# Kernel tuning notes

Measured on AMD Instinct MI355X. Metric: run time of the kernel, lower is better.

## Reference

```python
import jax, jax.numpy as jnp
import numpy as np

N = 100000      # num nodes
E = 1600000     # num edges (avg degree 16)
F_IN = 256      # num_node_features
HID = 128       # hid_dim
C = 16          # num_classes


def gcn_conv(x, W, b, src, dst, num_nodes):
    # Linear transform first (PyG GCNConv transforms then aggregates)
    h = x @ W  # [N, out]
    # Symmetric normalization with self-loops already included in src/dst
    ones = jnp.ones_like(dst, dtype=h.dtype)
    deg = jax.ops.segment_sum(ones, dst, num_segments=num_nodes)  # in-degree incl. self-loop
    dinv = jnp.where(deg > 0, jax.lax.rsqrt(deg), 0.0)
    norm = dinv[src] * dinv[dst]                 # [E+N]
    msg = h[src] * norm[:, None]                 # gather + scale
    out = jax.ops.segment_sum(msg, dst, num_segments=num_nodes)  # scatter-add
    return out + b


def setup_inputs() -> dict:
    key = jax.random.key(0)
    k = jax.random.split(key, 4)
    x = jax.random.normal(k[0], (N, F_IN), dtype=jnp.float32)
    edge_index = jax.random.randint(k[1], (2, E), 0, N, dtype=jnp.int32)
    W1 = jax.random.normal(k[2], (F_IN, HID), dtype=jnp.float32) * (1.0 / np.sqrt(F_IN))
    b1 = jnp.zeros((HID,), dtype=jnp.float32)
    W2 = jax.random.normal(k[3], (HID, C), dtype=jnp.float32) * (1.0 / np.sqrt(HID))
    b2 = jnp.zeros((C,), dtype=jnp.float32)
    return {"x": x, "edge_index": edge_index, "W1": W1, "b1": b1, "W2": W2, "b2": b2}


def reference(x, edge_index, W1, b1, W2, b2):
    num_nodes = x.shape[0]
    loop = jnp.arange(num_nodes, dtype=edge_index.dtype)
    src = jnp.concatenate([edge_index[0], loop])  # add self-loops
    dst = jnp.concatenate([edge_index[1], loop])
    h = gcn_conv(x, W1, b1, src, dst, num_nodes)
    h = jax.nn.relu(h)
    # F.dropout(training=self.training): identity in eval mode
    out = gcn_conv(h, W2, b2, src, dst, num_nodes)
    return out
```

## Files before the change

### kernel.cpp

```cpp
#include <hip/hip_runtime.h>
#include <cstddef>

#define CAP 48
#define NBUILD 4096

typedef short short8 __attribute__((ext_vector_type(8)));
typedef float floatx4 __attribute__((ext_vector_type(4)));

__device__ inline float b2f_lo(unsigned int u) {
  union { unsigned int i; float f; } c;
  c.i = u << 16;
  return c.f;
}
__device__ inline float b2f_hi(unsigned int u) {
  union { unsigned int i; float f; } c;
  c.i = u & 0xFFFF0000u;
  return c.f;
}
__device__ inline unsigned short f2b(float f) {
  union { float f; unsigned int i; } c;
  c.f = f;
  unsigned int u = c.i;
  unsigned int r = (u + 0x7FFFu + ((u >> 16) & 1u)) >> 16;
  return (unsigned short)r;
}
__device__ inline float dinv_of(int c) { return rsqrtf((float)(c + 1)); }

__global__ void k_prep(int* __restrict__ cnt, int N,
                       const float* __restrict__ W1, unsigned short* __restrict__ W1T) {
  int i = blockIdx.x * 256 + threadIdx.x;
  if (i < N) cnt[i] = 0;
  if (i < 256 * 128) {
    int k = i >> 7, n = i & 127;
    W1T[n * 256 + k] = f2b(W1[i]);
  }
}

__global__ __launch_bounds__(256) void k_build_gemm1(
    const int* __restrict__ src, const int* __restrict__ dst, int E, int N,
    int* __restrict__ cnt, int* __restrict__ bucket,
    const float* __restrict__ X, const unsigned short* __restrict__ W1T,
    unsigned short* __restrict__ H1, int M, int gblocks, int total) {
  __shared__ unsigned short As[64 * 40];
  __shared__ unsigned short Bs[128 * 40];

  const unsigned int idx = blockIdx.x;
  const unsigned int gBefore = (idx * (unsigned int)gblocks) / (unsigned int)total;
  const unsigned int gAfter = ((idx + 1) * (unsigned int)gblocks) / (unsigned int)total;
  const bool isGemm = (gAfter > gBefore);

  if (!isGemm) {
    const int bi = (int)(idx - gBefore);
    const int g = bi & 7;
    const int S = (N + 7) >> 3;
    const int lo = g * S;
    const int hi = min(N, lo + S);
    const int tb = (bi >> 3) * 256 + (int)threadIdx.x;
    const int T = (NBUILD >> 3) * 256;
    const int E4 = E & ~3;

    for (int i0 = tb * 4; i0 < E4; i0 += T * 4) {
      int4 d4 = *(const int4*)(dst + i0);
      int4 s4 = *(const int4*)(src + i0);
      int p0 = CAP, p1 = CAP, p2 = CAP, p3 = CAP;
      if (d4.x >= lo && d4.x < hi) p0 = atomicAdd(&cnt[d4.x], 1);
      if (d4.y >= lo && d4.y < hi) p1 = atomicAdd(&cnt[d4.y], 1);
      if (d4.z >= lo && d4.z < hi) p2 = atomicAdd(&cnt[d4.z], 1);
      if (d4.w >= lo && d4.w < hi) p3 = atomicAdd(&cnt[d4.w], 1);
      if (p0 < CAP) bucket[(size_t)d4.x * CAP + p0] = s4.x;
      if (p1 < CAP) bucket[(size_t)d4.y * CAP + p1] = s4.y;
      if (p2 < CAP) bucket[(size_t)d4.z * CAP + p2] = s4.z;
      if (p3 < CAP) bucket[(size_t)d4.w * CAP + p3] = s4.w;
    }
    if (tb < E - E4) {
      int i = E4 + tb;
      int d = dst[i], s = src[i];
      if (d >= lo && d < hi) {
        int pos = atomicAdd(&cnt[d], 1);
        if (pos < CAP) bucket[(size_t)d * CAP + pos] = s;
      }
    }
    return;
  }

  const int bid = (int)gBefore;
  const int tid = threadIdx.x;
  const int wave = tid >> 6;
  const int lane = tid & 63;
  const int quad = lane >> 4;
  const int l16 = lane & 15;
  const int row0 = bid * 64;
  const int n0 = wave * 32;

  floatx4 acc[4][2];
#pragma unroll
  for (int r = 0; r < 4; r++)
#pragma unroll
    for (int c = 0; c < 2; c++) acc[r][c] = (floatx4){0.f, 0.f, 0.f, 0.f};

  for (int k0 = 0; k0 < 256; k0 += 32) {
    {
      int r = tid >> 2;
      int q = tid & 3;
      int gr = row0 + r;
      float4 v0 = make_float4(0.f, 0.f, 0.f, 0.f), v1 = v0;
      if (gr < M) {
        const float4* xp = (const float4*)(X + (size_t)gr * 256 + k0 + q * 8);
        v0 = xp[0];
        v1 = xp[1];
      }
      unsigned short tmp[8];
      tmp[0] = f2b(v0.x); tmp[1] = f2b(v0.y); tmp[2] = f2b(v0.z); tmp[3] = f2b(v0.w);
      tmp[4] = f2b(v1.x); tmp[5] = f2b(v1.y); tmp[6] = f2b(v1.z); tmp[7] = f2b(v1.w);
      *(uint4*)(As + r * 40 + q * 8) = *(const uint4*)(tmp);
    }
    {
      int n = tid >> 1;
      int half = (tid & 1) * 16;
      const uint4* wp = (const uint4*)(W1T + (size_t)n * 256 + k0 + half);
      uint4 w0 = wp[0];
      uint4 w1 = wp[1];
      unsigned short* p = Bs + n * 40 + half;
      *(uint4*)(p) = w0;
      *(uint4*)(p + 8) = w1;
    }
    __syncthreads();

    short8 afr[4], bfr[2];
#pragma unroll
    for (int r = 0; r < 4; r++)
      afr[r] = *(const short8*)(As + (r * 16 + l16) * 40 + quad * 8);
#pragma unroll
    for (int c = 0; c < 2; c++)
      bfr[c] = *(const short8*)(Bs + (n0 + c * 16 + l16) * 40 + quad * 8);
#pragma unroll
    for (int r = 0; r < 4; r++)
#pragma unroll
      for (int c = 0; c < 2; c++)
        acc[r][c] = __builtin_amdgcn_mfma_f32_16x16x32_bf16(afr[r], bfr[c], acc[r][c], 0, 0, 0);
    __syncthreads();
  }

#pragma unroll
  for (int r = 0; r < 4; r++) {
#pragma unroll
    for (int c = 0; c < 2; c++) {
      int col = n0 + c * 16 + l16;
#pragma unroll
      for (int i = 0; i < 4; i++) {
        int gr = row0 + r * 16 + quad * 4 + i;
        if (gr < M) H1[(size_t)gr * 128 + col] = f2b(acc[r][c][i]);
      }
    }
  }
}

__global__ __launch_bounds__(256) void k_agg1g2(const unsigned short* __restrict__ H1,
                                                const int* __restrict__ cnt,
                                                const int* __restrict__ bucket,
                                                const float* __restrict__ b1,
                                                const float* __restrict__ W2,
                                                unsigned short* __restrict__ H2, int N) {
  __shared__ float Ws[16 * 130];
  {
    int t = threadIdx.x;
    if (t < 128) {
      const float4* s4 = (const float4*)(W2 + t * 16);
      float4 w0 = s4[0], w1 = s4[1], w2v = s4[2], w3 = s4[3];
      float* d = Ws + (t >> 3) * 130 + (t & 7) * 16;
      d[0] = w0.x;  d[1] = w0.y;  d[2] = w0.z;  d[3] = w0.w;
      d[4] = w1.x;  d[5] = w1.y;  d[6] = w1.z;  d[7] = w1.w;
      d[8] = w2v.x; d[9] = w2v.y; d[10] = w2v.z; d[11] = w2v.w;
      d[12] = w3.x; d[13] = w3.y; d[14] = w3.z; d[15] = w3.w;
    }
  }
  __syncthreads();

  const int lane = threadIdx.x & 15;
  const int node = blockIdx.x * 16 + (threadIdx.x >> 4);
  if (node >= N) return;
  const int cn = cnt[node];
  const float di = dinv_of(cn);
  const float wself = di * di;
  const int deg = min(cn, CAP);
  const int* bk = bucket + (size_t)node * CAP;

  int idx0 = (lane < deg) ? bk[lane] : 0;
  int idx1 = (lane + 16 < deg) ? bk[lane + 16] : 0;
  int idx2 = (lane + 32 < deg) ? bk[lane + 32] : 0;
  float dv0 = (lane < deg) ? dinv_of(cnt[idx0]) : 0.f;
  float dv1 = (lane + 16 < deg) ? dinv_of(cnt[idx1]) : 0.f;
  float dv2 = (lane + 32 < deg) ? dinv_of(cnt[idx2]) : 0.f;

  uint4 hs = ((const uint4*)(H1 + (size_t)node * 128))[lane];
  float a0 = b2f_lo(hs.x) * wself, a1 = b2f_hi(hs.x) * wself;
  float a2 = b2f_lo(hs.y) * wself, a3 = b2f_hi(hs.y) * wself;
  float a4 = b2f_lo(hs.z) * wself, a5 = b2f_hi(hs.z) * wself;
  float a6 = b2f_lo(hs.w) * wself, a7 = b2f_hi(hs.w) * wself;
  float c0 = 0.f, c1 = 0.f, c2 = 0.f, c3 = 0.f, c4 = 0.f, c5 = 0.f, c6 = 0.f, c7 = 0.f;

  for (int j = 0; j < deg; j += 4) {
    int b = j >> 4;
    int idxB = (b == 0) ? idx0 : ((b == 1) ? idx1 : idx2);
    float dvB = (b == 0) ? dv0 : ((b == 1) ? dv1 : dv2);
    int base = j & 15;
    int s0 = __shfl(idxB, base + 0, 16);
    int s1 = __shfl(idxB, base + 1, 16);
    int s2 = __shfl(idxB, base + 2, 16);
    int s3 = __shfl(idxB, base + 3, 16);
    float w0 = __shfl(dvB, base + 0, 16) * di;
    float w1 = __shfl(dvB, base + 1, 16) * di;
    float w2 = __shfl(dvB, base + 2, 16) * di;
    float w3 = __shfl(dvB, base + 3, 16) * di;
    uint4 v0 = ((const uint4*)(H1 + (size_t)s0 * 128))[lane];
    uint4 v1 = ((const uint4*)(H1 + (size_t)s1 * 128))[lane];
    uint4 v2 = ((const uint4*)(H1 + (size_t)s2 * 128))[lane];
    uint4 v3 = ((const uint4*)(H1 + (size_t)s3 * 128))[lane];
    a0 += b2f_lo(v0.x) * w0; a1 += b2f_hi(v0.x) * w0;
    a2 += b2f_lo(v0.y) * w0; a3 += b2f_hi(v0.y) * w0;
    a4 += b2f_lo(v0.z) * w0; a5 += b2f_hi(v0.z) * w0;
    a6 += b2f_lo(v0.w) * w0; a7 += b2f_hi(v0.w) * w0;
    c0 += b2f_lo(v1.x) * w1; c1 += b2f_hi(v1.x) * w1;
    c2 += b2f_lo(v1.y) * w1; c3 += b2f_hi(v1.y) * w1;
    c4 += b2f_lo(v1.z) * w1; c5 += b2f_hi(v1.z) * w1;
    c6 += b2f_lo(v1.w) * w1; c7 += b2f_hi(v1.w) * w1;
    a0 += b2f_lo(v2.x) * w2; a1 += b2f_hi(v2.x) * w2;
    a2 += b2f_lo(v2.y) * w2; a3 += b2f_hi(v2.y) * w2;
    a4 += b2f_lo(v2.z) * w2; a5 += b2f_hi(v2.z) * w2;
    a6 += b2f_lo(v2.w) * w2; a7 += b2f_hi(v2.w) * w2;
    a0 += b2f_lo(v3.x) * w3; a1 += b2f_hi(v3.x) * w3;
    a2 += b2f_lo(v3.y) * w3; a3 += b2f_hi(v3.y) * w3;
    a4 += b2f_lo(v3.z) * w3; a5 += b2f_hi(v3.z) * w3;
    a6 += b2f_lo(v3.w) * w3; a7 += b2f_hi(v3.w) * w3;
  }
  a0 += c0; a1 += c1; a2 += c2; a3 += c3;
  a4 += c4; a5 += c5; a6 += c6; a7 += c7;

  float4 bb0 = ((const float4*)b1)[lane * 2];
  float4 bb1 = ((const float4*)b1)[lane * 2 + 1];
  float av[8];
  av[0] = fmaxf(a0 + bb0.x, 0.f); av[1] = fmaxf(a1 + bb0.y, 0.f);
  av[2] = fmaxf(a2 + bb0.z, 0.f); av[3] = fmaxf(a3 + bb0.w, 0.f);
  av[4] = fmaxf(a4 + bb1.x, 0.f); av[5] = fmaxf(a5 + bb1.y, 0.f);
  av[6] = fmaxf(a6 + bb1.z, 0.f); av[7] = fmaxf(a7 + bb1.w, 0.f);

  float2 p2[8];
#pragma unroll
  for (int c = 0; c < 8; c++) p2[c] = make_float2(0.f, 0.f);
  const float* wl = Ws + lane * 130;
#pragma unroll
  for (int i = 0; i < 8; i++) {
    const float a = av[i];
    const float2* wr = (const float2*)(wl + i * 16);
#pragma unroll
    for (int c = 0; c < 8; c++) {
      float2 wv = wr[c];
      p2[c].x += a * wv.x;
      p2[c].y += a * wv.y;
    }
  }
  float p[16];
#pragma unroll
  for (int c = 0; c < 8; c++) { p[2 * c] = p2[c].x; p[2 * c + 1] = p2[c].y; }

  float k8[8];
  {
    const bool hi = (lane & 8) != 0;
#pragma unroll
    for (int i = 0; i < 8; i++) {
      float keep = hi ? p[8 + i] : p[i];
      float send = hi ? p[i] : p[8 + i];
      k8[i] = keep + __shfl_xor(send, 8, 16);
    }
  }
  float k4[4];
  {
    const bool hi = (lane & 4) != 0;
#pragma unroll
    for (int i = 0; i < 4; i++) {
      float keep = hi ? k8[4 + i] : k8[i];
      float send = hi ? k8[i] : k8[4 + i];
      k4[i] = keep + __shfl_xor(send, 4, 16);
    }
  }
  float k2[2];
  {
    const bool hi = (lane & 2) != 0;
#pragma unroll
    for (int i = 0; i < 2; i++) {
      float keep = hi ? k4[2 + i] : k4[i];
      float send = hi ? k4[i] : k4[2 + i];
      k2[i] = keep + __shfl_xor(send, 2, 16);
    }
  }
  float v;
  {
    const bool hi = (lane & 1) != 0;
    float keep = hi ? k2[1] : k2[0];
    float send = hi ? k2[0] : k2[1];
    v = keep + __shfl_xor(send, 1, 16);
  }
  H2[(size_t)node * 16 + lane] = f2b(v);
}

__global__ __launch_bounds__(256) void k_agg2(const unsigned short* __restrict__ H2,
                                              const int* __restrict__ cnt,
                                              const int* __restrict__ bucket,
                                              const float* __restrict__ b2,
                                              float* __restrict__ out, int N) {
  const int half = threadIdx.x & 1;
  const int node = blockIdx.x * 128 + (threadIdx.x >> 1);
  if (node >= N) return;
  const int cn = cnt[node];
  const float di = dinv_of(cn);
  const float wself = di * di;
  const int deg = min(cn, CAP);
  const int* bk = bucket + (size_t)node * CAP;

  uint4 h = ((const uint4*)(H2 + (size_t)node * 16))[half];
  float a0 = b2f_lo(h.x) * wself, a1 = b2f_hi(h.x) * wself;
  float a2 = b2f_lo(h.y) * wself, a3 = b2f_hi(h.y) * wself;
  float a4 = b2f_lo(h.z) * wself, a5 = b2f_hi(h.z) * wself;
  float a6 = b2f_lo(h.w) * wself, a7 = b2f_hi(h.w) * wself;

  for (int j = 0; j < deg; j += 4) {
    int4 s4 = *(const int4*)(bk + j);
    int s0 = s4.x;
    int s1 = (j + 1 < deg) ? s4.y : 0;
    int s2 = (j + 2 < deg) ? s4.z : 0;
    int s3 = (j + 3 < deg) ? s4.w : 0;
    float w0 = dinv_of(cnt[s0]) * di;
    float w1 = (j + 1 < deg) ? dinv_of(cnt[s1]) * di : 0.f;
    float w2 = (j + 2 < deg) ? dinv_of(cnt[s2]) * di : 0.f;
    float w3 = (j + 3 < deg) ? dinv_of(cnt[s3]) * di : 0.f;
    uint4 v0 = ((const uint4*)(H2 + (size_t)s0 * 16))[half];
    uint4 v1 = ((const uint4*)(H2 + (size_t)s1 * 16))[half];
    uint4 v2 = ((const uint4*)(H2 + (size_t)s2 * 16))[half];
    uint4 v3 = ((const uint4*)(H2 + (size_t)s3 * 16))[half];
    a0 += b2f_lo(v0.x) * w0 + b2f_lo(v1.x) * w1 + b2f_lo(v2.x) * w2 + b2f_lo(v3.x) * w3;
    a1 += b2f_hi(v0.x) * w0 + b2f_hi(v1.x) * w1 + b2f_hi(v2.x) * w2 + b2f_hi(v3.x) * w3;
    a2 += b2f_lo(v0.y) * w0 + b2f_lo(v1.y) * w1 + b2f_lo(v2.y) * w2 + b2f_lo(v3.y) * w3;
    a3 += b2f_hi(v0.y) * w0 + b2f_hi(v1.y) * w1 + b2f_hi(v2.y) * w2 + b2f_hi(v3.y) * w3;
    a4 += b2f_lo(v0.z) * w0 + b2f_lo(v1.z) * w1 + b2f_lo(v2.z) * w2 + b2f_lo(v3.z) * w3;
    a5 += b2f_hi(v0.z) * w0 + b2f_hi(v1.z) * w1 + b2f_hi(v2.z) * w2 + b2f_hi(v3.z) * w3;
    a6 += b2f_lo(v0.w) * w0 + b2f_lo(v1.w) * w1 + b2f_lo(v2.w) * w2 + b2f_lo(v3.w) * w3;
    a7 += b2f_hi(v0.w) * w0 + b2f_hi(v1.w) * w1 + b2f_hi(v2.w) * w2 + b2f_hi(v3.w) * w3;
  }

  float4 bb0 = ((const float4*)b2)[half * 2];
  float4 bb1 = ((const float4*)b2)[half * 2 + 1];
  float4 o0 = make_float4(a0 + bb0.x, a1 + bb0.y, a2 + bb0.z, a3 + bb0.w);
  float4 o1 = make_float4(a4 + bb1.x, a5 + bb1.y, a6 + bb1.z, a7 + bb1.w);
  ((float4*)(out + (size_t)node * 16))[half * 2] = o0;
  ((float4*)(out + (size_t)node * 16))[half * 2 + 1] = o1;
}


extern "C" void kernel_launch(void* const* d_in, const int* in_sizes, int n_in,
                              void* d_out, int out_size, void* d_ws, size_t ws_size,
                              hipStream_t stream) {
  const float* x  = (const float*)d_in[0];
  const int* eidx = (const int*)d_in[1];
  const float* W1 = (const float*)d_in[2];
  const float* b1 = (const float*)d_in[3];
  const float* W2 = (const float*)d_in[4];
  const float* b2 = (const float*)d_in[5];
  float* out = (float*)d_out;

  const int HID = in_sizes[3];
  const int F   = in_sizes[2] / HID;
  const int N   = in_sizes[0] / F;
  const int E   = in_sizes[1] / 2;
  (void)n_in; (void)out_size; (void)ws_size;

  const int* src = eidx;
  const int* dst = eidx + E;

  char* base = (char*)d_ws;
  size_t off = 0;
  auto alloc = [&](size_t bytes) -> char* {
    char* p = base + off;
    off = (off + bytes + 255) & ~(size_t)255;
    return p;
  };
  int*            cnt    = (int*)alloc((size_t)N * 4);
  int*            bucket = (int*)alloc((size_t)N * CAP * 4);
  unsigned short* w1t    = (unsigned short*)alloc((size_t)256 * 128 * 2);
  unsigned short* h1     = (unsigned short*)alloc((size_t)N * 128 * 2);
  unsigned short* h2     = (unsigned short*)alloc((size_t)N * 16 * 2);

  const int nbN = (N + 255) / 256;
  const int gblocks = (N + 63) / 64;
  const int total = NBUILD + gblocks;

  hipLaunchKernelGGL(k_prep, dim3(nbN), dim3(256), 0, stream, cnt, N, W1, w1t);
  hipLaunchKernelGGL(k_build_gemm1, dim3(total), dim3(256), 0, stream,
                     src, dst, E, N, cnt, bucket, x, w1t, h1, N, gblocks, total);
  hipLaunchKernelGGL(k_agg1g2, dim3((N + 15) / 16), dim3(256), 0, stream, h1, cnt, bucket,
                     b1, W2, h2, N);
  hipLaunchKernelGGL(k_agg2, dim3((N + 127) / 128), dim3(256), 0, stream, h2, cnt, bucket,
                     b2, out, N);
}
```

Baseline: 329.7 us.

## Drop range-partitioned bucket build; split layer-2 neighbor loop across lane pairs

The edge-bucketing part of the fused build/GEMM kernel no longer runs 8 passes over all edges with each pass filtering a destination range. Each thread now handles one group of four edges and issues atomics for all of them, which cuts redundant edge reads but gives up the locality of atomics and bucket writes within a range. The layer-2 aggregation now uses four threads per node instead of two: two parities split the neighbor list and their sums are combined with a shuffle. This doubles the grid and adds memory parallelism per node.

```diff
diff --git a/kernel.cpp b/kernel.cpp
--- a/kernel.cpp
+++ b/kernel.cpp
@@ -2,7 +2,6 @@
 #include <cstddef>
 
 #define CAP 48
-#define NBUILD 4096
 
 typedef short short8 __attribute__((ext_vector_type(8)));
 typedef float floatx4 __attribute__((ext_vector_type(4)));
@@ -51,31 +50,23 @@
 
   if (!isGemm) {
     const int bi = (int)(idx - gBefore);
-    const int g = bi & 7;
-    const int S = (N + 7) >> 3;
-    const int lo = g * S;
-    const int hi = min(N, lo + S);
-    const int tb = (bi >> 3) * 256 + (int)threadIdx.x;
-    const int T = (NBUILD >> 3) * 256;
-    const int E4 = E & ~3;
-
-    for (int i0 = tb * 4; i0 < E4; i0 += T * 4) {
+    const int tb = bi * 256 + (int)threadIdx.x;
+    const int i0 = tb * 4;
+    if (i0 >= E) return;
+    if (i0 + 3 < E) {
       int4 d4 = *(const int4*)(dst + i0);
       int4 s4 = *(const int4*)(src + i0);
-      int p0 = CAP, p1 = CAP, p2 = CAP, p3 = CAP;
-      if (d4.x >= lo && d4.x < hi) p0 = atomicAdd(&cnt[d4.x], 1);
-      if (d4.y >= lo && d4.y < hi) p1 = atomicAdd(&cnt[d4.y], 1);
-      if (d4.z >= lo && d4.z < hi) p2 = atomicAdd(&cnt[d4.z], 1);
-      if (d4.w >= lo && d4.w < hi) p3 = atomicAdd(&cnt[d4.w], 1);
+      int p0 = atomicAdd(&cnt[d4.x], 1);
+      int p1 = atomicAdd(&cnt[d4.y], 1);
+      int p2 = atomicAdd(&cnt[d4.z], 1);
+      int p3 = atomicAdd(&cnt[d4.w], 1);
       if (p0 < CAP) bucket[(size_t)d4.x * CAP + p0] = s4.x;
       if (p1 < CAP) bucket[(size_t)d4.y * CAP + p1] = s4.y;
       if (p2 < CAP) bucket[(size_t)d4.z * CAP + p2] = s4.z;
       if (p3 < CAP) bucket[(size_t)d4.w * CAP + p3] = s4.w;
-    }
-    if (tb < E - E4) {
-      int i = E4 + tb;
-      int d = dst[i], s = src[i];
-      if (d >= lo && d < hi) {
+    } else {
+      for (int i = i0; i < E; ++i) {
+        int d = dst[i], s = src[i];
         int pos = atomicAdd(&cnt[d], 1);
         if (pos < CAP) bucket[(size_t)d * CAP + pos] = s;
       }
@@ -308,8 +299,10 @@
                                               const int* __restrict__ bucket,
                                               const float* __restrict__ b2,
                                               float* __restrict__ out, int N) {
-  const int half = threadIdx.x & 1;
-  const int node = blockIdx.x * 128 + (threadIdx.x >> 1);
+  const int t = threadIdx.x;
+  const int half = t & 1;
+  const int par = (t >> 1) & 1;
+  const int node = blockIdx.x * 64 + (t >> 2);
   if (node >= N) return;
   const int cn = cnt[node];
   const float di = dinv_of(cn);
@@ -317,13 +310,16 @@
   const int deg = min(cn, CAP);
   const int* bk = bucket + (size_t)node * CAP;
 
-  uint4 h = ((const uint4*)(H2 + (size_t)node * 16))[half];
-  float a0 = b2f_lo(h.x) * wself, a1 = b2f_hi(h.x) * wself;
-  float a2 = b2f_lo(h.y) * wself, a3 = b2f_hi(h.y) * wself;
-  float a4 = b2f_lo(h.z) * wself, a5 = b2f_hi(h.z) * wself;
-  float a6 = b2f_lo(h.w) * wself, a7 = b2f_hi(h.w) * wself;
-
-  for (int j = 0; j < deg; j += 4) {
+  float a0 = 0.f, a1 = 0.f, a2 = 0.f, a3 = 0.f, a4 = 0.f, a5 = 0.f, a6 = 0.f, a7 = 0.f;
+  if (par == 0) {
+    uint4 h = ((const uint4*)(H2 + (size_t)node * 16))[half];
+    a0 = b2f_lo(h.x) * wself; a1 = b2f_hi(h.x) * wself;
+    a2 = b2f_lo(h.y) * wself; a3 = b2f_hi(h.y) * wself;
+    a4 = b2f_lo(h.z) * wself; a5 = b2f_hi(h.z) * wself;
+    a6 = b2f_lo(h.w) * wself; a7 = b2f_hi(h.w) * wself;
+  }
+
+  for (int j = par * 4; j < deg; j += 8) {
     int4 s4 = *(const int4*)(bk + j);
     int s0 = s4.x;
     int s1 = (j + 1 < deg) ? s4.y : 0;
@@ -347,12 +343,19 @@
     a7 += b2f_hi(v0.w) * w0 + b2f_hi(v1.w) * w1 + b2f_hi(v2.w) * w2 + b2f_hi(v3.w) * w3;
   }
 
-  float4 bb0 = ((const float4*)b2)[half * 2];
-  float4 bb1 = ((const float4*)b2)[half * 2 + 1];
-  float4 o0 = make_float4(a0 + bb0.x, a1 + bb0.y, a2 + bb0.z, a3 + bb0.w);
-  float4 o1 = make_float4(a4 + bb1.x, a5 + bb1.y, a6 + bb1.z, a7 + bb1.w);
-  ((float4*)(out + (size_t)node * 16))[half * 2] = o0;
-  ((float4*)(out + (size_t)node * 16))[half * 2 + 1] = o1;
+  a0 += __shfl_xor(a0, 2); a1 += __shfl_xor(a1, 2);
+  a2 += __shfl_xor(a2, 2); a3 += __shfl_xor(a3, 2);
+  a4 += __shfl_xor(a4, 2); a5 += __shfl_xor(a5, 2);
+  a6 += __shfl_xor(a6, 2); a7 += __shfl_xor(a7, 2);
+
+  if (par == 0) {
+    float4 bb0 = ((const float4*)b2)[half * 2];
+    float4 bb1 = ((const float4*)b2)[half * 2 + 1];
+    float4 o0 = make_float4(a0 + bb0.x, a1 + bb0.y, a2 + bb0.z, a3 + bb0.w);
+    float4 o1 = make_float4(a4 + bb1.x, a5 + bb1.y, a6 + bb1.z, a7 + bb1.w);
+    ((float4*)(out + (size_t)node * 16))[half * 2] = o0;
+    ((float4*)(out + (size_t)node * 16))[half * 2 + 1] = o1;
+  }
 }
 
 
@@ -391,13 +394,15 @@
 
   const int nbN = (N + 255) / 256;
   const int gblocks = (N + 63) / 64;
-  const int total = NBUILD + gblocks;
+  const int quads = (E + 3) / 4;
+  const int nbuild = (quads + 255) / 256;
+  const int total = nbuild + gblocks;
 
   hipLaunchKernelGGL(k_prep, dim3(nbN), dim3(256), 0, stream, cnt, N, W1, w1t);
   hipLaunchKernelGGL(k_build_gemm1, dim3(total), dim3(256), 0, stream,
                      src, dst, E, N, cnt, bucket, x, w1t, h1, N, gblocks, total);
   hipLaunchKernelGGL(k_agg1g2, dim3((N + 15) / 16), dim3(256), 0, stream, h1, cnt, bucket,
                      b1, W2, h2, N);
-  hipLaunchKernelGGL(k_agg2, dim3((N + 127) / 128), dim3(256), 0, stream, h2, cnt, bucket,
+  hipLaunchKernelGGL(k_agg2, dim3((N + 63) / 64), dim3(256), 0, stream, h2, cnt, bucket,
                      b2, out, N);
 }
```

After: 318.5 us. 1.04x faster.
